# Kernel tuning notes

Measured on AMD Instinct MI355X. Metric: run time of the kernel, lower is better.

## Reference

```python
import jax, jax.numpy as jnp
import numpy as np

B, N, D = 16, 1024, 128


def setup_inputs() -> dict:
    key = jax.random.key(0)
    ks = jax.random.split(key, 12)
    x = jax.random.normal(ks[0], (B, N, D), dtype=jnp.float32)
    # binary symmetric-ish adjacency mask (0/1 floats)
    adj = jax.random.randint(ks[1], (B, N, N), 0, 2).astype(jnp.float32)
    Ww = jax.random.normal(ks[2], (D, D), dtype=jnp.float32) * 0.05
    Wb = jax.random.normal(ks[3], (D,), dtype=jnp.float32) * 0.05
    A = jax.random.normal(ks[4], (D, D), dtype=jnp.float32) * 0.05
    wi_u = jax.random.normal(ks[5], (D,), dtype=jnp.float32) * 0.05
    wi_x = jax.random.normal(ks[6], (D,), dtype=jnp.float32) * 0.05
    wf_u = jax.random.normal(ks[7], (D,), dtype=jnp.float32) * 0.05
    wf_x = jax.random.normal(ks[8], (D,), dtype=jnp.float32) * 0.05
    wo_u = jax.random.normal(ks[9], (D,), dtype=jnp.float32) * 0.05
    wo_x = jax.random.normal(ks[10], (D,), dtype=jnp.float32) * 0.05
    return {"x": x, "adj": adj, "Ww": Ww, "Wb": Wb, "A": A,
            "wi_u": wi_u, "wi_x": wi_x, "wf_u": wf_u, "wf_x": wf_x,
            "wo_u": wo_u, "wo_x": wo_x}


def reference(x, adj, Ww, Wb, A, wi_u, wi_x, wf_u, wf_x, wo_u, wo_x):
    # h = W(x): [B,N,D]
    h = jnp.einsum('bnf,df->bnd', x, Ww) + Wb
    # e[b,j,k] = (h A) . h  -> symmetrized dense scores [B,N,N]
    e = jnp.einsum('bjl,bkl->bjk', jnp.einsum('bjd,dl->bjl', h, A), h)
    e = e + jnp.swapaxes(e, 1, 2)
    # masked softmax over axis=1 (columns), then re-mask by adj
    scores = jnp.where(adj > 0, e, 0.0)
    attention = jax.nn.softmax(scores, axis=1) * adj
    # aggregation
    h_prime = jax.nn.relu(jnp.einsum('bij,bjk->bik', attention, h))
    # LSTM-style gates: scalar per node, broadcast over features
    ic = jax.nn.sigmoid(h_prime @ wi_u + x @ wi_x)[..., None]
    fc = jax.nn.sigmoid(h_prime @ wf_u + x @ wf_x)[..., None]
    oc = jax.nn.sigmoid(h_prime @ wo_u + x @ wo_x)[..., None]
    return oc * jnp.tanh(ic * h_prime + fc * x)
```

## Files before the change

kernel.cpp:

```cpp
#include <hip/hip_runtime.h>


#define B_ 16
#define N_ 1024
#define D_ 128

typedef __attribute__((ext_vector_type(8))) short bf16x8;
typedef __attribute__((ext_vector_type(4))) float f32x4;

__device__ __forceinline__ float b2f(unsigned short u) {
    union { unsigned int i; float f; } v; v.i = ((unsigned int)u) << 16; return v.f;
}
__device__ __forceinline__ unsigned short f2b(float f) {
    union { float f; unsigned int i; } v; v.f = f;
    unsigned int x = v.i;
    return (unsigned short)((x + 0x7fffu + ((x >> 16) & 1u)) >> 16);
}
__device__ __forceinline__ float clamp60(float v) {
    return fminf(fmaxf(v, -60.f), 60.f);
}
__device__ __forceinline__ bf16x8 load8f(const float* p) {
    float4 a = *reinterpret_cast<const float4*>(p);
    float4 b = *reinterpret_cast<const float4*>(p + 4);
    bf16x8 v;
    v[0] = (short)f2b(a.x); v[1] = (short)f2b(a.y);
    v[2] = (short)f2b(a.z); v[3] = (short)f2b(a.w);
    v[4] = (short)f2b(b.x); v[5] = (short)f2b(b.y);
    v[6] = (short)f2b(b.z); v[7] = (short)f2b(b.w);
    return v;
}

__global__ __launch_bounds__(256) void k0_w2t(
    const float* __restrict__ Ww, const float* __restrict__ Wb,
    const float* __restrict__ A, unsigned short* __restrict__ WwB,
    unsigned short* __restrict__ W2T, float* __restrict__ wbA) {
    int t = blockIdx.x * 256 + threadIdx.x;
    int l = t >> 7, f = t & 127;
    float acc = 0.f;
    for (int d = 0; d < 128; ++d)
        acc += A[d * 128 + l] * Ww[d * 128 + f];
    W2T[l * 128 + f] = f2b(acc);
    WwB[t] = f2b(Ww[t]);
    if (blockIdx.x == 0 && threadIdx.x < 128) {
        float s = 0.f;
// ... 5 lines not shown
__global__ __launch_bounds__(256) void kmask(
    const float* __restrict__ adj, unsigned long long* __restrict__ maskJ) {
    int w = threadIdx.x >> 6, lane = threadIdx.x & 63;
    size_t base = ((size_t)blockIdx.x * 4 + w) * 256;
    unsigned long long w0 = __ballot(adj[base + 0 * 64 + lane] > 0.f);
    unsigned long long w1 = __ballot(adj[base + 1 * 64 + lane] > 0.f);
    unsigned long long w2 = __ballot(adj[base + 2 * 64 + lane] > 0.f);
    unsigned long long w3 = __ballot(adj[base + 3 * 64 + lane] > 0.f);
    unsigned long long o = lane == 0 ? w0 : lane == 1 ? w1 : lane == 2 ? w2 : w3;
    if (lane < 4) maskJ[(base >> 6) + lane] = o;
}

__global__ __launch_bounds__(256) void k1_hu(
    const float* __restrict__ x, const unsigned short* __restrict__ WwB,
    const float* __restrict__ Wb, const unsigned short* __restrict__ W2T,
    const float* __restrict__ wbA, const float* __restrict__ adj,
    unsigned short* __restrict__ h, unsigned short* __restrict__ u,
    unsigned short* __restrict__ hT, unsigned long long* __restrict__ maskJ) {
    __shared__ unsigned short lds[16][128];
    int w = threadIdx.x >> 6, lane = threadIdx.x & 63;
    int c = lane & 15, q = lane >> 4;
    int rowbase = blockIdx.x * 16;
    int b = rowbase >> 10;
    int n0 = rowbase & 1023;

    bf16x8 xa[4];
    const float* xrow = x + (size_t)(rowbase + c) * 128;
#pragma unroll
    for (int ks = 0; ks < 4; ++ks)
        xa[ks] = load8f(xrow + ks * 32 + q * 8);

#pragma unroll
    for (int tt = 0; tt < 2; ++tt) {
        int t = w * 2 + tt;
        f32x4 acch = {0.f, 0.f, 0.f, 0.f};
        f32x4 accu = {0.f, 0.f, 0.f, 0.f};
        const unsigned short* wwrow = WwB + (t * 16 + c) * 128;
        const unsigned short* w2row = W2T + (t * 16 + c) * 128;
#pragma unroll
        for (int ks = 0; ks < 4; ++ks) {
            bf16x8 bw = *reinterpret_cast<const bf16x8*>(wwrow + ks * 32 + q * 8);
            bf16x8 b2 = *reinterpret_cast<const bf16x8*>(w2row + ks * 32 + q * 8);
            acch = __builtin_amdgcn_mfma_f32_16x16x32_bf16(xa[ks], bw, acch, 0, 0, 0);
            accu = __builtin_amdgcn_mfma_f32_16x16x32_bf16(xa[ks], b2, accu, 0, 0, 0);
        }
        float wb = Wb[t * 16 + c];
        float ub = wbA[t * 16 + c];
#pragma unroll
        for (int r = 0; r < 4; ++r) {
            int row = rowbase + q * 4 + r;
            unsigned short hv = f2b(acch[r] + wb);
            unsigned short uv = f2b(accu[r] + ub);
            h[(size_t)row * 128 + t * 16 + c] = hv;
            u[(size_t)row * 128 + t * 16 + c] = uv;
            lds[q * 4 + r][t * 16 + c] = hv;
        }
    }

    {
        const float* adjb = adj + ((size_t)(rowbase + w * 4)) * 1024;
#pragma unroll
        for (int r = 0; r < 4; ++r) {
#pragma unroll
            for (int g = 0; g < 16; ++g) {
                unsigned long long m = __ballot(adjb[(size_t)r * 1024 + g * 64 + lane] > 0.f);
                if (lane == 0) maskJ[(size_t)(rowbase + w * 4 + r) * 16 + g] = m;
            }
        }
    }

    __syncthreads();
    int tid = threadIdx.x;
    if (tid < 128) {
        int d = tid;
        unsigned int p[8];
#pragma unroll
        for (int k = 0; k < 8; ++k) {
            unsigned int v0 = lds[2 * k][d], v1 = lds[2 * k + 1][d];
            p[k] = v0 | (v1 << 16);
        }
        size_t basehT = ((size_t)(b * 128 + d)) * 1024 + n0;
        uint4* dst = reinterpret_cast<uint4*>(hT + basehT);
        dst[0] = make_uint4(p[0], p[1], p[2], p[3]);
        dst[1] = make_uint4(p[4], p[5], p[6], p[7]);
    }
}


__global__ __launch_bounds__(256) void k2_scores(
    const unsigned short* __restrict__ h, const unsigned short* __restrict__ u,
    const unsigned long long* __restrict__ maskJ,
    unsigned short* __restrict__ att, float* __restrict__ colpart) {
    __shared__ unsigned long long lmask[32][16];
    int w = threadIdx.x >> 6, lane = threadIdx.x & 63;
    int c = lane & 15, q = lane >> 4;
    int b = blockIdx.x >> 5;
    int iblk = blockIdx.x & 31;
    int i0 = iblk * 32;
    const unsigned short* hb = h + (size_t)b * N_ * D_;
    const unsigned short* ub = u + (size_t)b * N_ * D_;

    {
        int tid = threadIdx.x;
        lmask[tid >> 4][tid & 15] =
            maskJ[(size_t)(b * 1024 + i0 + (tid >> 4)) * 16 + (tid & 15)];
        lmask[16 + (tid >> 4)][tid & 15] =
            maskJ[(size_t)(b * 1024 + i0 + 16 + (tid >> 4)) * 16 + (tid & 15)];
    }
    __syncthreads();

    bf16x8 Au0[4], Ah0[4], Au1[4], Ah1[4];
#pragma unroll
    for (int ks = 0; ks < 4; ++ks) {
        Au0[ks] = *reinterpret_cast<const bf16x8*>(ub + (i0 + c) * 128 + ks * 32 + q * 8);
        Ah0[ks] = *reinterpret_cast<const bf16x8*>(hb + (i0 + c) * 128 + ks * 32 + q * 8);
        Au1[ks] = *reinterpret_cast<const bf16x8*>(ub + (i0 + 16 + c) * 128 + ks * 32 + q * 8);
        Ah1[ks] = *reinterpret_cast<const bf16x8*>(hb + (i0 + 16 + c) * 128 + ks * 32 + q * 8);
    }
    unsigned short* attrow = att + ((size_t)(b * 1024 + i0)) * 1024;
    float* cprow = colpart + ((size_t)(b * 32 + iblk)) * 1024;

    int jt0 = w * 16;
#pragma unroll
    for (int t = 0; t < 16; ++t) {
        int jt = jt0 + t, j0 = jt * 16;
        bf16x8 Bh[4], Bu[4];
#pragma unroll
        for (int ks = 0; ks < 4; ++ks) {
            Bh[ks] = *reinterpret_cast<const bf16x8*>(hb + (j0 + c) * 128 + ks * 32 + q * 8);
            Bu[ks] = *reinterpret_cast<const bf16x8*>(ub + (j0 + c) * 128 + ks * 32 + q * 8);
        }
        f32x4 a00 = {0.f, 0.f, 0.f, 0.f};
        f32x4 a01 = {0.f, 0.f, 0.f, 0.f};
        f32x4 a10 = {0.f, 0.f, 0.f, 0.f};
        f32x4 a11 = {0.f, 0.f, 0.f, 0.f};
#pragma unroll
// ... 36 lines not shown
__global__ __launch_bounds__(256) void k3_gemm(
    const unsigned short* __restrict__ att, const float* __restrict__ rl0,
    const unsigned short* __restrict__ hT, const float* __restrict__ x,
    const float* __restrict__ wi_u, const float* __restrict__ wi_x,
    const float* __restrict__ wf_u, const float* __restrict__ wf_x,
    const float* __restrict__ wo_u, const float* __restrict__ wo_x,
    float* __restrict__ out) {
    __shared__ float red[4][16][129];
    int w = threadIdx.x >> 6, lane = threadIdx.x & 63;
    int c = lane & 15, q = lane >> 4;
    int b = blockIdx.x >> 6;
    int i0 = (blockIdx.x & 63) * 16;
    const unsigned short* attrow = att + ((size_t)(b * 1024 + i0 + c)) * 1024;
    const unsigned short* hTb = hT + (size_t)b * 128 * 1024;
    const float* rl0b = rl0 + b * 1024;

    f32x4 hp[8];
#pragma unroll
    for (int t = 0; t < 8; ++t) hp[t] = (f32x4){0.f, 0.f, 0.f, 0.f};

#pragma unroll
    for (int tt = 0; tt < 8; ++tt) {
        int jp = w * 8 + tt;
        int jb = jp * 32 + q * 8;
        bf16x8 eraw = *reinterpret_cast<const bf16x8*>(attrow + jb);
        float4 r0 = *reinterpret_cast<const float4*>(rl0b + jb);
        float4 r1 = *reinterpret_cast<const float4*>(rl0b + jb + 4);
        bf16x8 a;
        a[0] = (short)f2b(b2f((unsigned short)eraw[0]) * r0.x);
        a[1] = (short)f2b(b2f((unsigned short)eraw[1]) * r0.y);
        a[2] = (short)f2b(b2f((unsigned short)eraw[2]) * r0.z);
        a[3] = (short)f2b(b2f((unsigned short)eraw[3]) * r0.w);
        a[4] = (short)f2b(b2f((unsigned short)eraw[4]) * r1.x);
        a[5] = (short)f2b(b2f((unsigned short)eraw[5]) * r1.y);
        a[6] = (short)f2b(b2f((unsigned short)eraw[6]) * r1.z);
        a[7] = (short)f2b(b2f((unsigned short)eraw[7]) * r1.w);
#pragma unroll
        for (int t = 0; t < 8; ++t) {
            bf16x8 bt = *reinterpret_cast<const bf16x8*>(
                hTb + (size_t)(t * 16 + c) * 1024 + jp * 32 + q * 8);
            hp[t] = __builtin_amdgcn_mfma_f32_16x16x32_bf16(a, bt, hp[t], 0, 0, 0);
        }
    }

#pragma unroll
    for (int t = 0; t < 8; ++t)
#pragma unroll
        for (int r = 0; r < 4; ++r)
            red[w][q * 4 + r][t * 16 + c] = hp[t][r];
    __syncthreads();
    if (w != 0) return;

#pragma unroll
    for (int t = 0; t < 8; ++t)
#pragma unroll
        for (int r = 0; r < 4; ++r)
            hp[t][r] = red[0][q * 4 + r][t * 16 + c] + red[1][q * 4 + r][t * 16 + c]
                     + red[2][q * 4 + r][t * 16 + c] + red[3][q * 4 + r][t * 16 + c];

    float xv[8][4];
#pragma unroll
    for (int t = 0; t < 8; ++t)
#pragma unroll
        for (int r = 0; r < 4; ++r) {
            hp[t][r] = fmaxf(hp[t][r], 0.f);
            xv[t][r] = x[(size_t)(b * 1024 + i0 + q * 4 + r) * 128 + t * 16 + c];
        }
    float wiu[8], wix[8], wfu[8], wfx[8], wou[8], wox[8];
#pragma unroll
    for (int t = 0; t < 8; ++t) {
        wiu[t] = wi_u[t * 16 + c]; wix[t] = wi_x[t * 16 + c];
        wfu[t] = wf_u[t * 16 + c]; wfx[t] = wf_x[t * 16 + c];
        wou[t] = wo_u[t * 16 + c]; wox[t] = wo_x[t * 16 + c];
    }
#pragma unroll
    for (int r = 0; r < 4; ++r) {
        float zi = 0.f, zf = 0.f, zo = 0.f;
#pragma unroll
        for (int t = 0; t < 8; ++t) {
            zi += hp[t][r] * wiu[t] + xv[t][r] * wix[t];
            zf += hp[t][r] * wfu[t] + xv[t][r] * wfx[t];
            zo += hp[t][r] * wou[t] + xv[t][r] * wox[t];
        }
        zi += __shfl_xor(zi, 1, 64); zi += __shfl_xor(zi, 2, 64);
        zi += __shfl_xor(zi, 4, 64); zi += __shfl_xor(zi, 8, 64);
        zf += __shfl_xor(zf, 1, 64); zf += __shfl_xor(zf, 2, 64);
        zf += __shfl_xor(zf, 4, 64); zf += __shfl_xor(zf, 8, 64);
        zo += __shfl_xor(zo, 1, 64); zo += __shfl_xor(zo, 2, 64);
        zo += __shfl_xor(zo, 4, 64); zo += __shfl_xor(zo, 8, 64);
        float ic = 1.f / (1.f + __expf(-zi));
        float fc = 1.f / (1.f + __expf(-zf));
        float oc = 1.f / (1.f + __expf(-zo));
#pragma unroll
        for (int t = 0; t < 8; ++t) {
            float zz = ic * hp[t][r] + fc * xv[t][r];
            float th = 1.f - 2.f / (__expf(2.f * zz) + 1.f);
            out[(size_t)(b * 1024 + i0 + q * 4 + r) * 128 + t * 16 + c] = oc * th;
        }
    }
}

__global__ __launch_bounds__(256) void k1_hu_nb(
    const float* __restrict__ x, const unsigned short* __restrict__ WwB,
    const float* __restrict__ Wb, const unsigned short* __restrict__ W2T,
    const float* __restrict__ wbA,
    unsigned short* __restrict__ h, unsigned short* __restrict__ u,
    unsigned short* __restrict__ hT) {
    __shared__ unsigned short lds[16][128];
    int w = threadIdx.x >> 6, lane = threadIdx.x & 63;
    int c = lane & 15, q = lane >> 4;
    int rowbase = blockIdx.x * 16;
    int b = rowbase >> 10;
    int n0 = rowbase & 1023;
    bf16x8 xa[4];
    const float* xrow = x + (size_t)(rowbase + c) * 128;
#pragma unroll
    for (int ks = 0; ks < 4; ++ks)
        xa[ks] = load8f(xrow + ks * 32 + q * 8);
#pragma unroll
    for (int tt = 0; tt < 2; ++tt) {
        int t = w * 2 + tt;
        f32x4 acch = {0.f, 0.f, 0.f, 0.f};
        f32x4 accu = {0.f, 0.f, 0.f, 0.f};
        const unsigned short* wwrow = WwB + (t * 16 + c) * 128;
        const unsigned short* w2row = W2T + (t * 16 + c) * 128;
#pragma unroll
        for (int ks = 0; ks < 4; ++ks) {
            bf16x8 bw = *reinterpret_cast<const bf16x8*>(wwrow + ks * 32 + q * 8);
            bf16x8 b2 = *reinterpret_cast<const bf16x8*>(w2row + ks * 32 + q * 8);
            acch = __builtin_amdgcn_mfma_f32_16x16x32_bf16(xa[ks], bw, acch, 0, 0, 0);
            accu = __builtin_amdgcn_mfma_f32_16x16x32_bf16(xa[ks], b2, accu, 0, 0, 0);
        }
        float wb = Wb[t * 16 + c];
        float ub = wbA[t * 16 + c];
#pragma unroll
        for (int r = 0; r < 4; ++r) {
            int row = rowbase + q * 4 + r;
            unsigned short hv = f2b(acch[r] + wb);
            unsigned short uv = f2b(accu[r] + ub);
            h[(size_t)row * 128 + t * 16 + c] = hv;
            u[(size_t)row * 128 + t * 16 + c] = uv;
            lds[q * 4 + r][t * 16 + c] = hv;
        }
    }
    __syncthreads();
    int tid = threadIdx.x;
    if (tid < 128) {
        int d = tid;
        unsigned int p[8];
#pragma unroll
        for (int k = 0; k < 8; ++k) {
            unsigned int v0 = lds[2 * k][d], v1 = lds[2 * k + 1][d];
            p[k] = v0 | (v1 << 16);
        }
        size_t basehT = ((size_t)(b * 128 + d)) * 1024 + n0;
        uint4* dst = reinterpret_cast<uint4*>(hT + basehT);
        dst[0] = make_uint4(p[0], p[1], p[2], p[3]);
        dst[1] = make_uint4(p[4], p[5], p[6], p[7]);
    }
}

__global__ __launch_bounds__(256) void k2_stats(
    const unsigned short* __restrict__ h, const unsigned short* __restrict__ u,
    const unsigned long long* __restrict__ maskJ, float* __restrict__ rl0) {
    int w = threadIdx.x >> 6, lane = threadIdx.x & 63;
    int c = lane & 15, q = lane >> 4;
    int b = blockIdx.x >> 6;
    int j0 = (blockIdx.x & 63) * 16;
    const unsigned short* hb = h + (size_t)b * N_ * D_;
    const unsigned short* ub = u + (size_t)b * N_ * D_;
    bf16x8 Bh[4], Bu[4];
#pragma unroll
    for (int ks = 0; ks < 4; ++ks) {
        Bh[ks] = *reinterpret_cast<const bf16x8*>(hb + (j0 + c) * 128 + ks * 32 + q * 8);
        Bu[ks] = *reinterpret_cast<const bf16x8*>(ub + (j0 + c) * 128 + ks * 32 + q * 8);
    }
    float colsum = 0.f;
    const unsigned long long* mrow = maskJ + (size_t)b * 1024 * 16 + (j0 >> 6);
    int jb = j0 & 63;
    for (int it = w; it < 64; it += 4) {
        int i0 = it * 16;
        f32x4 acc = {0.f, 0.f, 0.f, 0.f};
#pragma unroll
        for (int ks = 0; ks < 4; ++ks) {
            bf16x8 au = *reinterpret_cast<const bf16x8*>(ub + (i0 + c) * 128 + ks * 32 + q * 8);
            bf16x8 ah = *reinterpret_cast<const bf16x8*>(hb + (i0 + c) * 128 + ks * 32 + q * 8);
            acc = __builtin_amdgcn_mfma_f32_16x16x32_bf16(au, Bh[ks], acc, 0, 0, 0);
            acc = __builtin_amdgcn_mfma_f32_16x16x32_bf16(ah, Bu[ks], acc, 0, 0, 0);
        }
#pragma unroll
        for (int r = 0; r < 4; ++r) {
            int i = i0 + q * 4 + r;
            unsigned long long mword = mrow[(size_t)i * 16];
            bool m = (mword >> (jb + c)) & 1ull;
            colsum += m ? __expf(clamp60(acc[r])) : 1.0f;
        }
    }
    colsum += __shfl_xor(colsum, 16, 64);
    colsum += __shfl_xor(colsum, 32, 64);
    __shared__ float part[4][16];
    if (lane < 16) part[w][lane] = colsum;
    __syncthreads();
    if (threadIdx.x < 16) {
        float s = part[0][threadIdx.x] + part[1][threadIdx.x]
                + part[2][threadIdx.x] + part[3][threadIdx.x];
        rl0[b * 1024 + j0 + threadIdx.x] = 1.0f / s;
    }
}

__global__ __launch_bounds__(256) void k3_fused(
    const unsigned short* __restrict__ h, const unsigned short* __restrict__ uu,
    const unsigned long long* __restrict__ maskJ, const float* __restrict__ rl0,
    const unsigned short* __restrict__ hT, const float* __restrict__ x,
    const float* __restrict__ wi_u, const float* __restrict__ wi_x,
    const float* __restrict__ wf_u, const float* __restrict__ wf_x,
    const float* __restrict__ wo_u, const float* __restrict__ wo_x,
    float* __restrict__ out) {
    __shared__ float red[4][16][129];
    int w = threadIdx.x >> 6, lane = threadIdx.x & 63;
    int c = lane & 15, q = lane >> 4;
    int b = blockIdx.x >> 6;
    int i0 = (blockIdx.x & 63) * 16;
    const unsigned short* hb = h + (size_t)b * N_ * D_;
    const unsigned short* ub = uu + (size_t)b * N_ * D_;
    const unsigned short* hTb = hT + (size_t)b * 128 * 1024;
    const unsigned long long* mrowI = maskJ + (size_t)(b * 1024 + i0 + c) * 16;
    const float* rl0b = rl0 + b * 1024;
    bf16x8 Bh[4], Bu[4];
#pragma unroll
    for (int ks = 0; ks < 4; ++ks) {
        Bh[ks] = *reinterpret_cast<const bf16x8*>(hb + (i0 + c) * 128 + ks * 32 + q * 8);
        Bu[ks] = *reinterpret_cast<const bf16x8*>(ub + (i0 + c) * 128 + ks * 32 + q * 8);
    }
    f32x4 hp[8];
#pragma unroll
    for (int t = 0; t < 8; ++t) hp[t] = (f32x4){0.f, 0.f, 0.f, 0.f};
    for (int jp = w; jp < 32; jp += 4) {
        int j0 = jp * 32;
        unsigned long long mw64 = mrowI[jp >> 1];
        unsigned int mbits = (unsigned int)(mw64 >> ((jp & 1) * 32));
        unsigned int u00, u01, u10, u11;
#pragma unroll
        for (int s = 0; s < 2; ++s) {
            int js = j0 + s * 16;
            f32x4 acc = {0.f, 0.f, 0.f, 0.f};
#pragma unroll
            for (int ks = 0; ks < 4; ++ks) {
                bf16x8 au = *reinterpret_cast<const bf16x8*>(ub + (js + c) * 128 + ks * 32 + q * 8);
                bf16x8 ah = *reinterpret_cast<const bf16x8*>(hb + (js + c) * 128 + ks * 32 + q * 8);
                acc = __builtin_amdgcn_mfma_f32_16x16x32_bf16(au, Bh[ks], acc, 0, 0, 0);
                acc = __builtin_amdgcn_mfma_f32_16x16x32_bf16(ah, Bu[ks], acc, 0, 0, 0);
            }
            float4 rv = *reinterpret_cast<const float4*>(rl0b + js + q * 4);
            int bb = s * 16 + q * 4;
            float a0 = ((mbits >> (bb + 0)) & 1u) ? __expf(clamp60(acc[0])) * rv.x : 0.f;
            float a1 = ((mbits >> (bb + 1)) & 1u) ? __expf(clamp60(acc[1])) * rv.y : 0.f;
            float a2 = ((mbits >> (bb + 2)) & 1u) ? __expf(clamp60(acc[2])) * rv.z : 0.f;
            float a3 = ((mbits >> (bb + 3)) & 1u) ? __expf(clamp60(acc[3])) * rv.w : 0.f;
            unsigned int p0 = (unsigned int)f2b(a0) | ((unsigned int)f2b(a1) << 16);
            unsigned int p1 = (unsigned int)f2b(a2) | ((unsigned int)f2b(a3) << 16);
            if (s == 0) { u00 = p0; u01 = p1; } else { u10 = p0; u11 = p1; }
        }
        int la = c + 32 * (q & 1);
        int lb = la + 16;
        unsigned int x0 = __shfl((int)u00, la, 64), x1 = __shfl((int)u01, la, 64);
        unsigned int x2 = __shfl((int)u00, lb, 64), x3 = __shfl((int)u01, lb, 64);
        unsigned int y0 = __shfl((int)u10, la, 64), y1 = __shfl((int)u11, la, 64);
        unsigned int y2 = __shfl((int)u10, lb, 64), y3 = __shfl((int)u11, lb, 64);
        bool hiq = (q >> 1) != 0;
        union { unsigned int ui[4]; bf16x8 v; } att;
        att.ui[0] = hiq ? y0 : x0;
        att.ui[1] = hiq ? y1 : x1;
        att.ui[2] = hiq ? y2 : x2;
        att.ui[3] = hiq ? y3 : x3;
#pragma unroll
        for (int t = 0; t < 8; ++t) {
            bf16x8 bt = *reinterpret_cast<const bf16x8*>(
                hTb + (size_t)(t * 16 + c) * 1024 + j0 + q * 8);
            hp[t] = __builtin_amdgcn_mfma_f32_16x16x32_bf16(att.v, bt, hp[t], 0, 0, 0);
        }
    }
#pragma unroll
    for (int t = 0; t < 8; ++t)
#pragma unroll
        for (int r = 0; r < 4; ++r)
            red[w][q * 4 + r][t * 16 + c] = hp[t][r];
    __syncthreads();
    if (w != 0) return;
#pragma unroll
    for (int t = 0; t < 8; ++t)
#pragma unroll
        for (int r = 0; r < 4; ++r)
            hp[t][r] = red[0][q * 4 + r][t * 16 + c] + red[1][q * 4 + r][t * 16 + c]
                     + red[2][q * 4 + r][t * 16 + c] + red[3][q * 4 + r][t * 16 + c];
// ... 44 lines not shown
                              hipStream_t stream) {
    const float* x    = (const float*)d_in[0];
    const float* adj  = (const float*)d_in[1];
    const float* Ww   = (const float*)d_in[2];
    const float* Wb   = (const float*)d_in[3];
    const float* A    = (const float*)d_in[4];
    const float* wi_u = (const float*)d_in[5];
    const float* wi_x = (const float*)d_in[6];
    const float* wf_u = (const float*)d_in[7];
    const float* wf_x = (const float*)d_in[8];
    const float* wo_u = (const float*)d_in[9];
    const float* wo_x = (const float*)d_in[10];
    float* out = (float*)d_out;
    char* ws = (char*)d_ws;

    if (ws_size >= (56ull << 20)) {
        unsigned short* WwB = (unsigned short*)(ws);
        unsigned short* W2T = (unsigned short*)(ws + (32u << 10));
        float* wbA          = (float*)(ws + (64u << 10));
        float* rl0          = (float*)(ws + (128u << 10));
        unsigned long long* maskJ = (unsigned long long*)(ws + (256u << 10));
        float* colpart      = (float*)(ws + (4ull << 20));
        unsigned short* h   = (unsigned short*)(ws + (8ull << 20));
        unsigned short* u   = (unsigned short*)(ws + (12ull << 20));
        unsigned short* hT  = (unsigned short*)(ws + (16ull << 20));
        unsigned short* att = (unsigned short*)(ws + (20ull << 20));

        k0_w2t<<<64, 256, 0, stream>>>(Ww, Wb, A, WwB, W2T, wbA);
        k1_hu<<<1024, 256, 0, stream>>>(x, WwB, Wb, W2T, wbA, adj, h, u, hT, maskJ);
        k2_scores<<<512, 256, 0, stream>>>(h, u, maskJ, att, colpart);
        k2b_recip<<<64, 256, 0, stream>>>(colpart, rl0);
        k3_gemm<<<1024, 256, 0, stream>>>(att, rl0, hT, x,
                                          wi_u, wi_x, wf_u, wf_x, wo_u, wo_x, out);
    } else {
        unsigned short* WwB = (unsigned short*)(ws);
        unsigned short* W2T = (unsigned short*)(ws + (32u << 10));
        float* wbA          = (float*)(ws + (64u << 10));
        float* rl0          = (float*)(ws + (128u << 10));
        unsigned short* h   = (unsigned short*)(ws + (1u << 20));
        unsigned short* u   = (unsigned short*)(ws + (5u << 20));
        unsigned short* hT  = (unsigned short*)(ws + (9u << 20));
        unsigned long long* maskJ = (unsigned long long*)(ws + (13u << 20));

        k0_w2t<<<64, 256, 0, stream>>>(Ww, Wb, A, WwB, W2T, wbA);
        kmask<<<16384, 256, 0, stream>>>(adj, maskJ);
        k1_hu_nb<<<1024, 256, 0, stream>>>(x, WwB, Wb, W2T, wbA, h, u, hT);
        k2_stats<<<1024, 256, 0, stream>>>(h, u, maskJ, rl0);
        k3_fused<<<1024, 256, 0, stream>>>(h, u, maskJ, rl0, hT, x,
                                           wi_u, wi_x, wf_u, wf_x, wo_u, wo_x, out);
    }
}
```

Baseline: 246.5 us.

## Fuse all stages into one cooperative persistent kernel with grid syncs

Replaces the five separate launches with a single cooperative kernel that runs each stage in a grid-stride loop, separated by grid-wide barriers. Column sums are accumulated with atomics instead of per-block partials plus a separate reduction kernel, and the mask is built in its own phase. The goal is to remove launch gaps and small reduction kernels, at the cost of grid-sync overhead, float atomic contention and an occupancy-limited grid size. The fallback paths now use a separate mask kernel and drop the older fused path.

```diff
diff --git a/kernel.cpp b/kernel.cpp
--- a/kernel.cpp
+++ b/kernel.cpp
@@ -1,4 +1,7 @@
 #include <hip/hip_runtime.h>
+#include <hip/hip_cooperative_groups.h>
+
+namespace cg = cooperative_groups;
 
 
 #define B_ 16
@@ -28,6 +31,278 @@
     v[4] = (short)f2b(b.x); v[5] = (short)f2b(b.y);
     v[6] = (short)f2b(b.z); v[7] = (short)f2b(b.w);
     return v;
+}
+
+struct MegaArgs {
+    const float *x, *adj, *Ww, *Wb, *A;
+    const float *wi_u, *wi_x, *wf_u, *wf_x, *wo_u, *wo_x;
+    float* out;
+    unsigned short *WwB, *W2T;
+    float *wbA, *colsum;
+    unsigned long long* maskJ;
+    unsigned short *h, *u, *hT, *att;
+};
+
+__global__ __launch_bounds__(256) void mega(MegaArgs a) {
+    cg::grid_group gg = cg::this_grid();
+    __shared__ __align__(16) unsigned char smem[33024];
+    int tid = threadIdx.x;
+    int w = tid >> 6, lane = tid & 63;
+    int c = lane & 15, q = lane >> 4;
+
+    for (int ub = blockIdx.x; ub < 64; ub += gridDim.x) {
+        int t = ub * 256 + tid;
+        int l = t >> 7, f = t & 127;
+        float acc = 0.f;
+        for (int d = 0; d < 128; ++d)
+            acc += a.A[d * 128 + l] * a.Ww[d * 128 + f];
+        a.W2T[l * 128 + f] = f2b(acc);
+        a.WwB[t] = f2b(a.Ww[t]);
+        a.colsum[t] = 0.f;
+        if (ub == 0 && tid < 128) {
+            float s = 0.f;
+            for (int d = 0; d < 128; ++d) s += a.Wb[d] * a.A[d * 128 + tid];
+            a.wbA[tid] = s;
+        }
+    }
+    for (int ub = blockIdx.x; ub < 4096; ub += gridDim.x) {
+        size_t base = ((size_t)ub * 4 + w) * 1024;
+        float v[16];
+#pragma unroll
+        for (int k = 0; k < 16; ++k) v[k] = a.adj[base + (size_t)k * 64 + lane];
+        unsigned long long m[16];
+#pragma unroll
+        for (int k = 0; k < 16; ++k) m[k] = __ballot(v[k] > 0.f);
+        unsigned long long mv = 0;
+#pragma unroll
+        for (int k = 0; k < 16; ++k) if (lane == k) mv = m[k];
+        if (lane < 16) a.maskJ[(base >> 6) + lane] = mv;
+    }
+    gg.sync();
+
+    {
+        auto lds1 = reinterpret_cast<unsigned short(*)[128]>(smem);
+        for (int blk = blockIdx.x; blk < 1024; blk += gridDim.x) {
+            int rowbase = blk * 16;
+            int b = rowbase >> 10;
+            int n0 = rowbase & 1023;
+            bf16x8 xa[4];
+            const float* xrow = a.x + (size_t)(rowbase + c) * 128;
+#pragma unroll
+            for (int ks = 0; ks < 4; ++ks)
+                xa[ks] = load8f(xrow + ks * 32 + q * 8);
+#pragma unroll
+            for (int tt = 0; tt < 2; ++tt) {
+                int t = w * 2 + tt;
+                f32x4 acch = {0.f, 0.f, 0.f, 0.f};
+                f32x4 accu = {0.f, 0.f, 0.f, 0.f};
+                const unsigned short* wwrow = a.WwB + (t * 16 + c) * 128;
+                const unsigned short* w2row = a.W2T + (t * 16 + c) * 128;
+#pragma unroll
+                for (int ks = 0; ks < 4; ++ks) {
+                    bf16x8 bw = *reinterpret_cast<const bf16x8*>(wwrow + ks * 32 + q * 8);
+                    bf16x8 b2 = *reinterpret_cast<const bf16x8*>(w2row + ks * 32 + q * 8);
+                    acch = __builtin_amdgcn_mfma_f32_16x16x32_bf16(xa[ks], bw, acch, 0, 0, 0);
+                    accu = __builtin_amdgcn_mfma_f32_16x16x32_bf16(xa[ks], b2, accu, 0, 0, 0);
+                }
+                float wb = a.Wb[t * 16 + c];
+                float ub2 = a.wbA[t * 16 + c];
+#pragma unroll
+                for (int r = 0; r < 4; ++r) {
+                    int row = rowbase + q * 4 + r;
+                    unsigned short hv = f2b(acch[r] + wb);
+                    unsigned short uv = f2b(accu[r] + ub2);
+                    a.h[(size_t)row * 128 + t * 16 + c] = hv;
+                    a.u[(size_t)row * 128 + t * 16 + c] = uv;
+                    lds1[q * 4 + r][t * 16 + c] = hv;
+                }
+            }
+            __syncthreads();
+            if (tid < 128) {
+                int d = tid;
+                unsigned int p[8];
+#pragma unroll
+                for (int k = 0; k < 8; ++k) {
+                    unsigned int v0 = lds1[2 * k][d], v1 = lds1[2 * k + 1][d];
+                    p[k] = v0 | (v1 << 16);
+                }
+                size_t basehT = ((size_t)(b * 128 + d)) * 1024 + n0;
+                uint4* dst = reinterpret_cast<uint4*>(a.hT + basehT);
+                dst[0] = make_uint4(p[0], p[1], p[2], p[3]);
+                dst[1] = make_uint4(p[4], p[5], p[6], p[7]);
+            }
+            __syncthreads();
+        }
+    }
+    gg.sync();
+
+    {
+        auto lmask = reinterpret_cast<unsigned long long(*)[8]>(smem);
+        for (int blk = blockIdx.x; blk < 1024; blk += gridDim.x) {
+            int b = blk >> 6, rem = blk & 63;
+            int iblk = rem >> 1, jh = rem & 1;
+            int i0 = iblk * 32, jbase = jh * 512;
+            const unsigned short* hb = a.h + (size_t)b * N_ * D_;
+            const unsigned short* ub2 = a.u + (size_t)b * N_ * D_;
+
+            lmask[tid >> 3][tid & 7] =
+                a.maskJ[(size_t)(b * 1024 + i0 + (tid >> 3)) * 16 + (jbase >> 6) + (tid & 7)];
+            __syncthreads();
+
+            bf16x8 Au0[4], Ah0[4], Au1[4], Ah1[4];
+#pragma unroll
+            for (int ks = 0; ks < 4; ++ks) {
+                Au0[ks] = *reinterpret_cast<const bf16x8*>(ub2 + (i0 + c) * 128 + ks * 32 + q * 8);
+                Ah0[ks] = *reinterpret_cast<const bf16x8*>(hb + (i0 + c) * 128 + ks * 32 + q * 8);
+                Au1[ks] = *reinterpret_cast<const bf16x8*>(ub2 + (i0 + 16 + c) * 128 + ks * 32 + q * 8);
+                Ah1[ks] = *reinterpret_cast<const bf16x8*>(hb + (i0 + 16 + c) * 128 + ks * 32 + q * 8);
+            }
+            unsigned short* attrow = a.att + ((size_t)(b * 1024 + i0)) * 1024;
+            float* csb = a.colsum + b * 1024;
+
+            int lt0 = w * 8;
+#pragma unroll
+            for (int t = 0; t < 8; ++t) {
+                int lt = lt0 + t;
+                int j0 = jbase + lt * 16;
+                bf16x8 Bh[4], Bu[4];
+#pragma unroll
+                for (int ks = 0; ks < 4; ++ks) {
+                    Bh[ks] = *reinterpret_cast<const bf16x8*>(hb + (j0 + c) * 128 + ks * 32 + q * 8);
+                    Bu[ks] = *reinterpret_cast<const bf16x8*>(ub2 + (j0 + c) * 128 + ks * 32 + q * 8);
+                }
+                f32x4 a00 = {0.f, 0.f, 0.f, 0.f};
+                f32x4 a01 = {0.f, 0.f, 0.f, 0.f};
+                f32x4 a10 = {0.f, 0.f, 0.f, 0.f};
+                f32x4 a11 = {0.f, 0.f, 0.f, 0.f};
+#pragma unroll
+                for (int ks = 0; ks < 4; ++ks) {
+                    a00 = __builtin_amdgcn_mfma_f32_16x16x32_bf16(Au0[ks], Bh[ks], a00, 0, 0, 0);
+                    a01 = __builtin_amdgcn_mfma_f32_16x16x32_bf16(Ah0[ks], Bu[ks], a01, 0, 0, 0);
+                    a10 = __builtin_amdgcn_mfma_f32_16x16x32_bf16(Au1[ks], Bh[ks], a10, 0, 0, 0);
+                    a11 = __builtin_amdgcn_mfma_f32_16x16x32_bf16(Ah1[ks], Bu[ks], a11, 0, 0, 0);
+                }
+                int wd = lt >> 2, sh = (lt & 3) * 16;
+                float colp = 0.f;
+#pragma unroll
+                for (int r = 0; r < 4; ++r) {
+                    float e0 = a00[r] + a01[r];
+                    float e1 = a10[r] + a11[r];
+                    bool m0 = (lmask[q * 4 + r][wd] >> (sh + c)) & 1ull;
+                    bool m1 = (lmask[16 + q * 4 + r][wd] >> (sh + c)) & 1ull;
+                    float ex0 = m0 ? __expf(clamp60(e0)) : 0.f;
+                    float ex1 = m1 ? __expf(clamp60(e1)) : 0.f;
+                    colp += (m0 ? ex0 : 1.0f) + (m1 ? ex1 : 1.0f);
+                    attrow[(size_t)(q * 4 + r) * 1024 + j0 + c] = f2b(ex0);
+                    attrow[(size_t)(16 + q * 4 + r) * 1024 + j0 + c] = f2b(ex1);
+                }
+                colp += __shfl_xor(colp, 16, 64);
+                colp += __shfl_xor(colp, 32, 64);
+                if (q == 0) atomicAdd(&csb[j0 + c], colp);
+            }
+            __syncthreads();
+        }
+    }
+    gg.sync();
+
+    for (int g2 = blockIdx.x * 256 + tid; g2 < 16384; g2 += gridDim.x * 256)
+        a.colsum[g2] = 1.0f / a.colsum[g2];
+    gg.sync();
+
+    {
+        auto red = reinterpret_cast<float(*)[16][129]>(smem);
+        for (int blk = blockIdx.x; blk < 1024; blk += gridDim.x) {
+            int b = blk >> 6;
+            int i0 = (blk & 63) * 16;
+            const unsigned short* attrow = a.att + ((size_t)(b * 1024 + i0 + c)) * 1024;
+            const unsigned short* hTb = a.hT + (size_t)b * 128 * 1024;
+            const float* rl0b = a.colsum + b * 1024;
+
+            f32x4 hp[8];
+#pragma unroll
+            for (int t = 0; t < 8; ++t) hp[t] = (f32x4){0.f, 0.f, 0.f, 0.f};
+
+#pragma unroll
+            for (int tt = 0; tt < 8; ++tt) {
+                int jp = w * 8 + tt;
+                int jb = jp * 32 + q * 8;
+                bf16x8 eraw = *reinterpret_cast<const bf16x8*>(attrow + jb);
+                float4 r0 = *reinterpret_cast<const float4*>(rl0b + jb);
+                float4 r1 = *reinterpret_cast<const float4*>(rl0b + jb + 4);
+                bf16x8 av;
+                av[0] = (short)f2b(b2f((unsigned short)eraw[0]) * r0.x);
+                av[1] = (short)f2b(b2f((unsigned short)eraw[1]) * r0.y);
+                av[2] = (short)f2b(b2f((unsigned short)eraw[2]) * r0.z);
+                av[3] = (short)f2b(b2f((unsigned short)eraw[3]) * r0.w);
+                av[4] = (short)f2b(b2f((unsigned short)eraw[4]) * r1.x);
+                av[5] = (short)f2b(b2f((unsigned short)eraw[5]) * r1.y);
+                av[6] = (short)f2b(b2f((unsigned short)eraw[6]) * r1.z);
+                av[7] = (short)f2b(b2f((unsigned short)eraw[7]) * r1.w);
+#pragma unroll
+                for (int t = 0; t < 8; ++t) {
+                    bf16x8 bt = *reinterpret_cast<const bf16x8*>(
+                        hTb + (size_t)(t * 16 + c) * 1024 + jp * 32 + q * 8);
+                    hp[t] = __builtin_amdgcn_mfma_f32_16x16x32_bf16(av, bt, hp[t], 0, 0, 0);
+                }
+            }
+
+#pragma unroll
+            for (int t = 0; t < 8; ++t)
+#pragma unroll
+                for (int r = 0; r < 4; ++r)
+                    red[w][q * 4 + r][t * 16 + c] = hp[t][r];
+            __syncthreads();
+            if (w == 0) {
+#pragma unroll
+                for (int t = 0; t < 8; ++t)
+#pragma unroll
+                    for (int r = 0; r < 4; ++r)
+                        hp[t][r] = red[0][q * 4 + r][t * 16 + c] + red[1][q * 4 + r][t * 16 + c]
+                                 + red[2][q * 4 + r][t * 16 + c] + red[3][q * 4 + r][t * 16 + c];
+                float xv[8][4];
+#pragma unroll
+                for (int t = 0; t < 8; ++t)
+#pragma unroll
+                    for (int r = 0; r < 4; ++r) {
+                        hp[t][r] = fmaxf(hp[t][r], 0.f);
+                        xv[t][r] = a.x[(size_t)(b * 1024 + i0 + q * 4 + r) * 128 + t * 16 + c];
+                    }
+                float wiu[8], wix[8], wfu[8], wfx[8], wou[8], wox[8];
+#pragma unroll
+                for (int t = 0; t < 8; ++t) {
+                    wiu[t] = a.wi_u[t * 16 + c]; wix[t] = a.wi_x[t * 16 + c];
+                    wfu[t] = a.wf_u[t * 16 + c]; wfx[t] = a.wf_x[t * 16 + c];
+                    wou[t] = a.wo_u[t * 16 + c]; wox[t] = a.wo_x[t * 16 + c];
+                }
+#pragma unroll
+                for (int r = 0; r < 4; ++r) {
+                    float zi = 0.f, zf = 0.f, zo = 0.f;
+#pragma unroll
+                    for (int t = 0; t < 8; ++t) {
+                        zi += hp[t][r] * wiu[t] + xv[t][r] * wix[t];
+                        zf += hp[t][r] * wfu[t] + xv[t][r] * wfx[t];
+                        zo += hp[t][r] * wou[t] + xv[t][r] * wox[t];
+                    }
+                    zi += __shfl_xor(zi, 1, 64); zi += __shfl_xor(zi, 2, 64);
+                    zi += __shfl_xor(zi, 4, 64); zi += __shfl_xor(zi, 8, 64);
+                    zf += __shfl_xor(zf, 1, 64); zf += __shfl_xor(zf, 2, 64);
+                    zf += __shfl_xor(zf, 4, 64); zf += __shfl_xor(zf, 8, 64);
+                    zo += __shfl_xor(zo, 1, 64); zo += __shfl_xor(zo, 2, 64);
+                    zo += __shfl_xor(zo, 4, 64); zo += __shfl_xor(zo, 8, 64);
+                    float ic = 1.f / (1.f + __expf(-zi));
+                    float fc = 1.f / (1.f + __expf(-zf));
+                    float oc = 1.f / (1.f + __expf(-zo));
+#pragma unroll
+                    for (int t = 0; t < 8; ++t) {
+                        float zz = ic * hp[t][r] + fc * xv[t][r];
+                        float th = 1.f - 2.f / (__expf(2.f * zz) + 1.f);
+                        a.out[(size_t)(b * 1024 + i0 + q * 4 + r) * 128 + t * 16 + c] = oc * th;
+                    }
+                }
+            }
+            __syncthreads();
+        }
+    }
 }
 
 __global__ __launch_bounds__(256) void k0_w2t(
@@ -63,22 +338,20 @@
 __global__ __launch_bounds__(256) void k1_hu(
     const float* __restrict__ x, const unsigned short* __restrict__ WwB,
     const float* __restrict__ Wb, const unsigned short* __restrict__ W2T,
-    const float* __restrict__ wbA, const float* __restrict__ adj,
+    const float* __restrict__ wbA,
     unsigned short* __restrict__ h, unsigned short* __restrict__ u,
-    unsigned short* __restrict__ hT, unsigned long long* __restrict__ maskJ) {
+    unsigned short* __restrict__ hT) {
     __shared__ unsigned short lds[16][128];
     int w = threadIdx.x >> 6, lane = threadIdx.x & 63;
     int c = lane & 15, q = lane >> 4;
     int rowbase = blockIdx.x * 16;
     int b = rowbase >> 10;
     int n0 = rowbase & 1023;
-
     bf16x8 xa[4];
     const float* xrow = x + (size_t)(rowbase + c) * 128;
 #pragma unroll
     for (int ks = 0; ks < 4; ++ks)
         xa[ks] = load8f(xrow + ks * 32 + q * 8);
-
 #pragma unroll
     for (int tt = 0; tt < 2; ++tt) {
         int t = w * 2 + tt;
@@ -105,19 +378,6 @@
             lds[q * 4 + r][t * 16 + c] = hv;
         }
     }
-
-    {
-        const float* adjb = adj + ((size_t)(rowbase + w * 4)) * 1024;
-#pragma unroll
-        for (int r = 0; r < 4; ++r) {
-#pragma unroll
-            for (int g = 0; g < 16; ++g) {
-                unsigned long long m = __ballot(adjb[(size_t)r * 1024 + g * 64 + lane] > 0.f);
-                if (lane == 0) maskJ[(size_t)(rowbase + w * 4 + r) * 16 + g] = m;
-            }
-        }
-    }
-
     __syncthreads();
     int tid = threadIdx.x;
     if (tid < 128) {
@@ -134,7 +394,6 @@
         dst[1] = make_uint4(p[4], p[5], p[6], p[7]);
     }
 }
-
 
 __global__ __launch_bounds__(256) void k2_scores(
     const unsigned short* __restrict__ h, const unsigned short* __restrict__ u,
@@ -148,7 +407,6 @@
     int i0 = iblk * 32;
     const unsigned short* hb = h + (size_t)b * N_ * D_;
     const unsigned short* ub = u + (size_t)b * N_ * D_;
-
     {
         int tid = threadIdx.x;
         lmask[tid >> 4][tid & 15] =
@@ -157,7 +415,6 @@
             maskJ[(size_t)(b * 1024 + i0 + 16 + (tid >> 4)) * 16 + (tid & 15)];
     }
     __syncthreads();
-
     bf16x8 Au0[4], Ah0[4], Au1[4], Ah1[4];
 #pragma unroll
     for (int ks = 0; ks < 4; ++ks) {
@@ -168,7 +425,6 @@
     }
     unsigned short* attrow = att + ((size_t)(b * 1024 + i0)) * 1024;
     float* cprow = colpart + ((size_t)(b * 32 + iblk)) * 1024;
-
     int jt0 = w * 16;
 #pragma unroll
     for (int t = 0; t < 16; ++t) {
@@ -235,11 +491,9 @@
     const unsigned short* attrow = att + ((size_t)(b * 1024 + i0 + c)) * 1024;
     const unsigned short* hTb = hT + (size_t)b * 128 * 1024;
     const float* rl0b = rl0 + b * 1024;
-
     f32x4 hp[8];
 #pragma unroll
     for (int t = 0; t < 8; ++t) hp[t] = (f32x4){0.f, 0.f, 0.f, 0.f};
-
 #pragma unroll
     for (int tt = 0; tt < 8; ++tt) {
         int jp = w * 8 + tt;
@@ -247,258 +501,20 @@
         bf16x8 eraw = *reinterpret_cast<const bf16x8*>(attrow + jb);
         float4 r0 = *reinterpret_cast<const float4*>(rl0b + jb);
         float4 r1 = *reinterpret_cast<const float4*>(rl0b + jb + 4);
-        bf16x8 a;
-        a[0] = (short)f2b(b2f((unsigned short)eraw[0]) * r0.x);
-        a[1] = (short)f2b(b2f((unsigned short)eraw[1]) * r0.y);
-        a[2] = (short)f2b(b2f((unsigned short)eraw[2]) * r0.z);
-        a[3] = (short)f2b(b2f((unsigned short)eraw[3]) * r0.w);
-        a[4] = (short)f2b(b2f((unsigned short)eraw[4]) * r1.x);
-        a[5] = (short)f2b(b2f((unsigned short)eraw[5]) * r1.y);
-        a[6] = (short)f2b(b2f((unsigned short)eraw[6]) * r1.z);
-        a[7] = (short)f2b(b2f((unsigned short)eraw[7]) * r1.w);
+        bf16x8 av;
+        av[0] = (short)f2b(b2f((unsigned short)eraw[0]) * r0.x);
+        av[1] = (short)f2b(b2f((unsigned short)eraw[1]) * r0.y);
+        av[2] = (short)f2b(b2f((unsigned short)eraw[2]) * r0.z);
+        av[3] = (short)f2b(b2f((unsigned short)eraw[3]) * r0.w);
+        av[4] = (short)f2b(b2f((unsigned short)eraw[4]) * r1.x);
+        av[5] = (short)f2b(b2f((unsigned short)eraw[5]) * r1.y);
+        av[6] = (short)f2b(b2f((unsigned short)eraw[6]) * r1.z);
+        av[7] = (short)f2b(b2f((unsigned short)eraw[7]) * r1.w);
 #pragma unroll
         for (int t = 0; t < 8; ++t) {
             bf16x8 bt = *reinterpret_cast<const bf16x8*>(
                 hTb + (size_t)(t * 16 + c) * 1024 + jp * 32 + q * 8);
-            hp[t] = __builtin_amdgcn_mfma_f32_16x16x32_bf16(a, bt, hp[t], 0, 0, 0);
-        }
-    }
-
-#pragma unroll
-    for (int t = 0; t < 8; ++t)
-#pragma unroll
-        for (int r = 0; r < 4; ++r)
-            red[w][q * 4 + r][t * 16 + c] = hp[t][r];
-    __syncthreads();
-    if (w != 0) return;
-
-#pragma unroll
-    for (int t = 0; t < 8; ++t)
-#pragma unroll
-        for (int r = 0; r < 4; ++r)
-            hp[t][r] = red[0][q * 4 + r][t * 16 + c] + red[1][q * 4 + r][t * 16 + c]
-                     + red[2][q * 4 + r][t * 16 + c] + red[3][q * 4 + r][t * 16 + c];
-
-    float xv[8][4];
-#pragma unroll
-    for (int t = 0; t < 8; ++t)
-#pragma unroll
-        for (int r = 0; r < 4; ++r) {
-            hp[t][r] = fmaxf(hp[t][r], 0.f);
-            xv[t][r] = x[(size_t)(b * 1024 + i0 + q * 4 + r) * 128 + t * 16 + c];
-        }
-    float wiu[8], wix[8], wfu[8], wfx[8], wou[8], wox[8];
-#pragma unroll
-    for (int t = 0; t < 8; ++t) {
-        wiu[t] = wi_u[t * 16 + c]; wix[t] = wi_x[t * 16 + c];
-        wfu[t] = wf_u[t * 16 + c]; wfx[t] = wf_x[t * 16 + c];
-        wou[t] = wo_u[t * 16 + c]; wox[t] = wo_x[t * 16 + c];
-    }
-#pragma unroll
-    for (int r = 0; r < 4; ++r) {
-        float zi = 0.f, zf = 0.f, zo = 0.f;
-#pragma unroll
-        for (int t = 0; t < 8; ++t) {
-            zi += hp[t][r] * wiu[t] + xv[t][r] * wix[t];
-            zf += hp[t][r] * wfu[t] + xv[t][r] * wfx[t];
-            zo += hp[t][r] * wou[t] + xv[t][r] * wox[t];
-        }
-        zi += __shfl_xor(zi, 1, 64); zi += __shfl_xor(zi, 2, 64);
-        zi += __shfl_xor(zi, 4, 64); zi += __shfl_xor(zi, 8, 64);
-        zf += __shfl_xor(zf, 1, 64); zf += __shfl_xor(zf, 2, 64);
-        zf += __shfl_xor(zf, 4, 64); zf += __shfl_xor(zf, 8, 64);
-        zo += __shfl_xor(zo, 1, 64); zo += __shfl_xor(zo, 2, 64);
-        zo += __shfl_xor(zo, 4, 64); zo += __shfl_xor(zo, 8, 64);
-        float ic = 1.f / (1.f + __expf(-zi));
-        float fc = 1.f / (1.f + __expf(-zf));
-        float oc = 1.f / (1.f + __expf(-zo));
-#pragma unroll
-        for (int t = 0; t < 8; ++t) {
-            float zz = ic * hp[t][r] + fc * xv[t][r];
-            float th = 1.f - 2.f / (__expf(2.f * zz) + 1.f);
-            out[(size_t)(b * 1024 + i0 + q * 4 + r) * 128 + t * 16 + c] = oc * th;
-        }
-    }
-}
-
-__global__ __launch_bounds__(256) void k1_hu_nb(
-    const float* __restrict__ x, const unsigned short* __restrict__ WwB,
-    const float* __restrict__ Wb, const unsigned short* __restrict__ W2T,
-    const float* __restrict__ wbA,
-    unsigned short* __restrict__ h, unsigned short* __restrict__ u,
-    unsigned short* __restrict__ hT) {
-    __shared__ unsigned short lds[16][128];
-    int w = threadIdx.x >> 6, lane = threadIdx.x & 63;
-    int c = lane & 15, q = lane >> 4;
-    int rowbase = blockIdx.x * 16;
-    int b = rowbase >> 10;
-    int n0 = rowbase & 1023;
-    bf16x8 xa[4];
-    const float* xrow = x + (size_t)(rowbase + c) * 128;
-#pragma unroll
-    for (int ks = 0; ks < 4; ++ks)
-        xa[ks] = load8f(xrow + ks * 32 + q * 8);
-#pragma unroll
-    for (int tt = 0; tt < 2; ++tt) {
-        int t = w * 2 + tt;
-        f32x4 acch = {0.f, 0.f, 0.f, 0.f};
-        f32x4 accu = {0.f, 0.f, 0.f, 0.f};
-        const unsigned short* wwrow = WwB + (t * 16 + c) * 128;
-        const unsigned short* w2row = W2T + (t * 16 + c) * 128;
-#pragma unroll
-        for (int ks = 0; ks < 4; ++ks) {
-            bf16x8 bw = *reinterpret_cast<const bf16x8*>(wwrow + ks * 32 + q * 8);
-            bf16x8 b2 = *reinterpret_cast<const bf16x8*>(w2row + ks * 32 + q * 8);
-            acch = __builtin_amdgcn_mfma_f32_16x16x32_bf16(xa[ks], bw, acch, 0, 0, 0);
-            accu = __builtin_amdgcn_mfma_f32_16x16x32_bf16(xa[ks], b2, accu, 0, 0, 0);
-        }
-        float wb = Wb[t * 16 + c];
-        float ub = wbA[t * 16 + c];
-#pragma unroll
-        for (int r = 0; r < 4; ++r) {
-            int row = rowbase + q * 4 + r;
-            unsigned short hv = f2b(acch[r] + wb);
-            unsigned short uv = f2b(accu[r] + ub);
-            h[(size_t)row * 128 + t * 16 + c] = hv;
-            u[(size_t)row * 128 + t * 16 + c] = uv;
-            lds[q * 4 + r][t * 16 + c] = hv;
-        }
-    }
-    __syncthreads();
-    int tid = threadIdx.x;
-    if (tid < 128) {
-        int d = tid;
-        unsigned int p[8];
-#pragma unroll
-        for (int k = 0; k < 8; ++k) {
-            unsigned int v0 = lds[2 * k][d], v1 = lds[2 * k + 1][d];
-            p[k] = v0 | (v1 << 16);
-        }
-        size_t basehT = ((size_t)(b * 128 + d)) * 1024 + n0;
-        uint4* dst = reinterpret_cast<uint4*>(hT + basehT);
-        dst[0] = make_uint4(p[0], p[1], p[2], p[3]);
-        dst[1] = make_uint4(p[4], p[5], p[6], p[7]);
-    }
-}
-
-__global__ __launch_bounds__(256) void k2_stats(
-    const unsigned short* __restrict__ h, const unsigned short* __restrict__ u,
-    const unsigned long long* __restrict__ maskJ, float* __restrict__ rl0) {
-    int w = threadIdx.x >> 6, lane = threadIdx.x & 63;
-    int c = lane & 15, q = lane >> 4;
-    int b = blockIdx.x >> 6;
-    int j0 = (blockIdx.x & 63) * 16;
-    const unsigned short* hb = h + (size_t)b * N_ * D_;
-    const unsigned short* ub = u + (size_t)b * N_ * D_;
-    bf16x8 Bh[4], Bu[4];
-#pragma unroll
-    for (int ks = 0; ks < 4; ++ks) {
-        Bh[ks] = *reinterpret_cast<const bf16x8*>(hb + (j0 + c) * 128 + ks * 32 + q * 8);
-        Bu[ks] = *reinterpret_cast<const bf16x8*>(ub + (j0 + c) * 128 + ks * 32 + q * 8);
-    }
-    float colsum = 0.f;
-    const unsigned long long* mrow = maskJ + (size_t)b * 1024 * 16 + (j0 >> 6);
-    int jb = j0 & 63;
-    for (int it = w; it < 64; it += 4) {
-        int i0 = it * 16;
-        f32x4 acc = {0.f, 0.f, 0.f, 0.f};
-#pragma unroll
-        for (int ks = 0; ks < 4; ++ks) {
-            bf16x8 au = *reinterpret_cast<const bf16x8*>(ub + (i0 + c) * 128 + ks * 32 + q * 8);
-            bf16x8 ah = *reinterpret_cast<const bf16x8*>(hb + (i0 + c) * 128 + ks * 32 + q * 8);
-            acc = __builtin_amdgcn_mfma_f32_16x16x32_bf16(au, Bh[ks], acc, 0, 0, 0);
-            acc = __builtin_amdgcn_mfma_f32_16x16x32_bf16(ah, Bu[ks], acc, 0, 0, 0);
-        }
-#pragma unroll
-        for (int r = 0; r < 4; ++r) {
-            int i = i0 + q * 4 + r;
-            unsigned long long mword = mrow[(size_t)i * 16];
-            bool m = (mword >> (jb + c)) & 1ull;
-            colsum += m ? __expf(clamp60(acc[r])) : 1.0f;
-        }
-    }
-    colsum += __shfl_xor(colsum, 16, 64);
-    colsum += __shfl_xor(colsum, 32, 64);
-    __shared__ float part[4][16];
-    if (lane < 16) part[w][lane] = colsum;
-    __syncthreads();
-    if (threadIdx.x < 16) {
-        float s = part[0][threadIdx.x] + part[1][threadIdx.x]
-                + part[2][threadIdx.x] + part[3][threadIdx.x];
-        rl0[b * 1024 + j0 + threadIdx.x] = 1.0f / s;
-    }
-}
-
-__global__ __launch_bounds__(256) void k3_fused(
-    const unsigned short* __restrict__ h, const unsigned short* __restrict__ uu,
-    const unsigned long long* __restrict__ maskJ, const float* __restrict__ rl0,
-    const unsigned short* __restrict__ hT, const float* __restrict__ x,
-    const float* __restrict__ wi_u, const float* __restrict__ wi_x,
-    const float* __restrict__ wf_u, const float* __restrict__ wf_x,
-    const float* __restrict__ wo_u, const float* __restrict__ wo_x,
-    float* __restrict__ out) {
-    __shared__ float red[4][16][129];
-    int w = threadIdx.x >> 6, lane = threadIdx.x & 63;
-    int c = lane & 15, q = lane >> 4;
-    int b = blockIdx.x >> 6;
-    int i0 = (blockIdx.x & 63) * 16;
-    const unsigned short* hb = h + (size_t)b * N_ * D_;
-    const unsigned short* ub = uu + (size_t)b * N_ * D_;
-    const unsigned short* hTb = hT + (size_t)b * 128 * 1024;
-    const unsigned long long* mrowI = maskJ + (size_t)(b * 1024 + i0 + c) * 16;
-    const float* rl0b = rl0 + b * 1024;
-    bf16x8 Bh[4], Bu[4];
-#pragma unroll
-    for (int ks = 0; ks < 4; ++ks) {
-        Bh[ks] = *reinterpret_cast<const bf16x8*>(hb + (i0 + c) * 128 + ks * 32 + q * 8);
-        Bu[ks] = *reinterpret_cast<const bf16x8*>(ub + (i0 + c) * 128 + ks * 32 + q * 8);
-    }
-    f32x4 hp[8];
-#pragma unroll
-    for (int t = 0; t < 8; ++t) hp[t] = (f32x4){0.f, 0.f, 0.f, 0.f};
-    for (int jp = w; jp < 32; jp += 4) {
-        int j0 = jp * 32;
-        unsigned long long mw64 = mrowI[jp >> 1];
-        unsigned int mbits = (unsigned int)(mw64 >> ((jp & 1) * 32));
-        unsigned int u00, u01, u10, u11;
-#pragma unroll
-        for (int s = 0; s < 2; ++s) {
-            int js = j0 + s * 16;
-            f32x4 acc = {0.f, 0.f, 0.f, 0.f};
-#pragma unroll
-            for (int ks = 0; ks < 4; ++ks) {
-                bf16x8 au = *reinterpret_cast<const bf16x8*>(ub + (js + c) * 128 + ks * 32 + q * 8);
-                bf16x8 ah = *reinterpret_cast<const bf16x8*>(hb + (js + c) * 128 + ks * 32 + q * 8);
-                acc = __builtin_amdgcn_mfma_f32_16x16x32_bf16(au, Bh[ks], acc, 0, 0, 0);
-                acc = __builtin_amdgcn_mfma_f32_16x16x32_bf16(ah, Bu[ks], acc, 0, 0, 0);
-            }
-            float4 rv = *reinterpret_cast<const float4*>(rl0b + js + q * 4);
-            int bb = s * 16 + q * 4;
-            float a0 = ((mbits >> (bb + 0)) & 1u) ? __expf(clamp60(acc[0])) * rv.x : 0.f;
-            float a1 = ((mbits >> (bb + 1)) & 1u) ? __expf(clamp60(acc[1])) * rv.y : 0.f;
-            float a2 = ((mbits >> (bb + 2)) & 1u) ? __expf(clamp60(acc[2])) * rv.z : 0.f;
-            float a3 = ((mbits >> (bb + 3)) & 1u) ? __expf(clamp60(acc[3])) * rv.w : 0.f;
-            unsigned int p0 = (unsigned int)f2b(a0) | ((unsigned int)f2b(a1) << 16);
-            unsigned int p1 = (unsigned int)f2b(a2) | ((unsigned int)f2b(a3) << 16);
-            if (s == 0) { u00 = p0; u01 = p1; } else { u10 = p0; u11 = p1; }
-        }
-        int la = c + 32 * (q & 1);
-        int lb = la + 16;
-        unsigned int x0 = __shfl((int)u00, la, 64), x1 = __shfl((int)u01, la, 64);
-        unsigned int x2 = __shfl((int)u00, lb, 64), x3 = __shfl((int)u01, lb, 64);
-        unsigned int y0 = __shfl((int)u10, la, 64), y1 = __shfl((int)u11, la, 64);
-        unsigned int y2 = __shfl((int)u10, lb, 64), y3 = __shfl((int)u11, lb, 64);
-        bool hiq = (q >> 1) != 0;
-        union { unsigned int ui[4]; bf16x8 v; } att;
-        att.ui[0] = hiq ? y0 : x0;
-        att.ui[1] = hiq ? y1 : x1;
-        att.ui[2] = hiq ? y2 : x2;
-        att.ui[3] = hiq ? y3 : x3;
-#pragma unroll
-        for (int t = 0; t < 8; ++t) {
-            bf16x8 bt = *reinterpret_cast<const bf16x8*>(
-                hTb + (size_t)(t * 16 + c) * 1024 + j0 + q * 8);
-            hp[t] = __builtin_amdgcn_mfma_f32_16x16x32_bf16(att.v, bt, hp[t], 0, 0, 0);
+            hp[t] = __builtin_amdgcn_mfma_f32_16x16x32_bf16(av, bt, hp[t], 0, 0, 0);
         }
     }
 #pragma unroll
@@ -573,39 +589,60 @@
     float* out = (float*)d_out;
     char* ws = (char*)d_ws;
 
-    if (ws_size >= (56ull << 20)) {
-        unsigned short* WwB = (unsigned short*)(ws);
-        unsigned short* W2T = (unsigned short*)(ws + (32u << 10));
-        float* wbA          = (float*)(ws + (64u << 10));
-        float* rl0          = (float*)(ws + (128u << 10));
-        unsigned long long* maskJ = (unsigned long long*)(ws + (256u << 10));
-        float* colpart      = (float*)(ws + (4ull << 20));
-        unsigned short* h   = (unsigned short*)(ws + (8ull << 20));
-        unsigned short* u   = (unsigned short*)(ws + (12ull << 20));
-        unsigned short* hT  = (unsigned short*)(ws + (16ull << 20));
-        unsigned short* att = (unsigned short*)(ws + (20ull << 20));
-
+    unsigned short* WwB = (unsigned short*)(ws);
+    unsigned short* W2T = (unsigned short*)(ws + (32u << 10));
+    float* wbA          = (float*)(ws + (64u << 10));
+    float* rl0          = (float*)(ws + (128u << 10));
+    unsigned long long* maskJ = (unsigned long long*)(ws + (256u << 10));
+    float* colpart      = (float*)(ws + (4ull << 20));
+    unsigned short* h   = (unsigned short*)(ws + (8ull << 20));
+    unsigned short* u   = (unsigned short*)(ws + (12ull << 20));
+    unsigned short* hT  = (unsigned short*)(ws + (16ull << 20));
+    unsigned short* att = (unsigned short*)(ws + (20ull << 20));
+
+    static int coopGrid = -1;
+    if (coopGrid < 0) {
+        coopGrid = 0;
+        hipDeviceProp_t prop;
+        if (hipGetDeviceProperties(&prop, 0) == hipSuccess && prop.cooperativeLaunch) {
+            int maxB = 0;
+            if (hipOccupancyMaxActiveBlocksPerMultiprocessor(
+                    &maxB, (const void*)mega, 256, 0) == hipSuccess && maxB > 0) {
+                long g = (long)prop.multiProcessorCount * maxB;
+                coopGrid = (int)(g > 1024 ? 1024 : g);
+            }
+        }
+    }
+
+    if (ws_size >= (56ull << 20) && coopGrid >= 256) {
+        MegaArgs ma;
+        ma.x = x; ma.adj = adj; ma.Ww = Ww; ma.Wb = Wb; ma.A = A;
+        ma.wi_u = wi_u; ma.wi_x = wi_x; ma.wf_u = wf_u; ma.wf_x = wf_x;
+        ma.wo_u = wo_u; ma.wo_x = wo_x; ma.out = out;
+        ma.WwB = WwB; ma.W2T = W2T; ma.wbA = wbA; ma.colsum = rl0;
+        ma.maskJ = maskJ; ma.h = h; ma.u = u; ma.hT = hT; ma.att = att;
+        void* args[] = {&ma};
+        hipLaunchCooperativeKernel((const void*)mega, dim3(coopGrid), dim3(256),
+                                   args, 0, stream);
+    } else if (ws_size >= (56ull << 20)) {
         k0_w2t<<<64, 256, 0, stream>>>(Ww, Wb, A, WwB, W2T, wbA);
-        k1_hu<<<1024, 256, 0, stream>>>(x, WwB, Wb, W2T, wbA, adj, h, u, hT, maskJ);
+        kmask<<<16384, 256, 0, stream>>>(adj, maskJ);
+        k1_hu<<<1024, 256, 0, stream>>>(x, WwB, Wb, W2T, wbA, h, u, hT);
         k2_scores<<<512, 256, 0, stream>>>(h, u, maskJ, att, colpart);
         k2b_recip<<<64, 256, 0, stream>>>(colpart, rl0);
         k3_gemm<<<1024, 256, 0, stream>>>(att, rl0, hT, x,
                                           wi_u, wi_x, wf_u, wf_x, wo_u, wo_x, out);
     } else {
-        unsigned short* WwB = (unsigned short*)(ws);
-        unsigned short* W2T = (unsigned short*)(ws + (32u << 10));
-        float* wbA          = (float*)(ws + (64u << 10));
-        float* rl0          = (float*)(ws + (128u << 10));
-        unsigned short* h   = (unsigned short*)(ws + (1u << 20));
-        unsigned short* u   = (unsigned short*)(ws + (5u << 20));
-        unsigned short* hT  = (unsigned short*)(ws + (9u << 20));
-        unsigned long long* maskJ = (unsigned long long*)(ws + (13u << 20));
-
+        unsigned short* h2   = (unsigned short*)(ws + (5ull << 20));
+        unsigned short* u2   = (unsigned short*)(ws + (9ull << 20));
+        unsigned short* hT2  = (unsigned short*)(ws + (13ull << 20));
+        unsigned short* att2 = (unsigned short*)(ws + (17ull << 20));
         k0_w2t<<<64, 256, 0, stream>>>(Ww, Wb, A, WwB, W2T, wbA);
         kmask<<<16384, 256, 0, stream>>>(adj, maskJ);
-        k1_hu_nb<<<1024, 256, 0, stream>>>(x, WwB, Wb, W2T, wbA, h, u, hT);
-        k2_stats<<<1024, 256, 0, stream>>>(h, u, maskJ, rl0);
-        k3_fused<<<1024, 256, 0, stream>>>(h, u, maskJ, rl0, hT, x,
-                                           wi_u, wi_x, wf_u, wf_x, wo_u, wo_x, out);
-    }
-}
+        k1_hu<<<1024, 256, 0, stream>>>(x, WwB, Wb, W2T, wbA, h2, u2, hT2);
+        k2_scores<<<512, 256, 0, stream>>>(h2, u2, maskJ, att2, colpart);
+        k2b_recip<<<64, 256, 0, stream>>>(colpart, rl0);
+        k3_gemm<<<1024, 256, 0, stream>>>(att2, rl0, hT2, x,
+                                          wi_u, wi_x, wf_u, wf_x, wo_u, wo_x, out);
+    }
+}
```

Measured after the change: 223.6 us. 1.1x faster.
